# Optimization experiments

Hardware: AMD Instinct MI355X
Metric: run time of the kernel (lower is better)

The kernel has to match this reference:

```python
import jax, jax.numpy as jnp
import numpy as np

B, K, C = 8192, 64, 8  # batch, feature dim, number of private-attribute classes


def setup_inputs() -> dict:
    key = jax.random.key(0)
    k1, k2, k3 = jax.random.split(key, 3)
    mu = jax.random.normal(k1, (B, K), dtype=jnp.float32)
    private_attribute = jax.random.randint(k2, (B,), 0, C)
    A = jax.random.normal(k3, (K, K), dtype=jnp.float32) * 0.05
    cov = A @ A.T + jnp.eye(K, dtype=jnp.float32)  # SPD prior covariance
    return {"mu": mu, "private_attribute": private_attribute, "cov": cov}


def _kldiv(mu1, S1, mu2, S2, k):
    # KL( N(mu1,S1) || N(mu2,S2) )
    d = mu2 - mu1
    tr = jnp.trace(jnp.linalg.solve(S2, S1))       # tr(inv(S2) S1)
    quad = d @ jnp.linalg.solve(S2, d)             # d^T inv(S2) d
    ld2 = jnp.linalg.slogdet(S2)[1]
    ld1 = jnp.linalg.slogdet(S1)[1]
    return 0.5 * (tr + quad - k + ld2 - ld1)


def reference(mu, private_attribute, cov):
    Bn, k = mu.shape
    labels = private_attribute
    ones = jnp.ones((Bn,), mu.dtype)
    counts = jax.ops.segment_sum(ones, labels, num_segments=C)                # [C]
    safe = jnp.maximum(counts, 1.0)
    mu_F = jax.ops.segment_sum(mu, labels, num_segments=C) / safe[:, None]    # [C,k] group means
    mu_total = jnp.mean(mu, axis=0)                                           # [k]
    dt = mu - mu_total
    Sigma_total = cov + dt.T @ dt / Bn                                        # [k,k]
    dc = mu - mu_F[labels]                                                    # [B,k]
    outer = jnp.einsum('bi,bj->bij', dc, dc)                                  # [B,k,k]
    Sigma_F = cov + jax.ops.segment_sum(outer, labels, num_segments=C) / safe[:, None, None]  # [C,k,k]
    kl = jax.vmap(lambda m, S: _kldiv(m, S, mu_total, Sigma_total, k))(mu_F, Sigma_F)  # [C]
    # The original loops `for i in range(len(keys)-1)` over dict keys ordered by
    # first occurrence in the batch, i.e. it SKIPS the class whose first sample
    # appears latest. Reproduce that exactly.
    pos = jnp.arange(Bn)
    first_pos = jnp.min(
        jnp.where(labels[:, None] == jnp.arange(C)[None, :], pos[:, None], Bn), axis=0
    )                                                                          # [C]
    present = first_pos < Bn
    last_key = jnp.argmax(jnp.where(present, first_pos, -1))
    w = jnp.where(present & (jnp.arange(C) != last_key), counts, 0.0)          # count_Fs weights
    result = jnp.sum(kl * w * Bn) / (Bn ** 2)
    return result
```

## Files before the change

kernel.cpp:

```cpp
#include <hip/hip_runtime.h>

#define CC 8
#define KK 64
#define BB 8192
#define NCHUNK 16
#define ROWS_PER_CHUNK (BB / NCHUNK)

#define OFF_G       0
#define OFF_GSUM    262144
#define OFF_GCOUNT  264192
#define OFF_GFIRST  264224
#define OFF_INV     264256
#define OFF_LOG     297024
#define OFF_L       297096
#define OFF_LDI     329864
#define OFF_X       330376
#define OFF_GPART   363144

__global__ __launch_bounds__(256) void gram_stats_kernel(
    const float* __restrict__ mu, const int* __restrict__ labels,
    float* __restrict__ Gpart, float* __restrict__ gsum,
    int* __restrict__ gcount, int* __restrict__ gfirst) {
  int c = blockIdx.y;
  int chunk = blockIdx.x;
  int tid = threadIdx.x;
  int lane = tid & 63, w = tid >> 6;
  int tx = tid & 15, ty = tid >> 4;
  __shared__ float rows[64][KK];
  __shared__ int labs[64];
  __shared__ float ssum[KK];
  double acc[4][4] = {{0.0}};
  float rsum = 0.f;
  int cnt = 0, first = BB;
  int base = chunk * ROWS_PER_CHUNK;
  const float4* mu4 = (const float4*)mu + (size_t)base * (KK / 4);

  if (tid < KK) ssum[tid] = 0.f;

  float4 pf[4];
  int plab = 0;
#pragma unroll
  for (int i = 0; i < 4; ++i) pf[i] = mu4[tid + i * 256];
  if (tid < 64) plab = labels[base + tid];

#pragma unroll 1
  for (int g = 0; g < ROWS_PER_CHUNK / 64; ++g) {
    __syncthreads();
    float4* rows4 = (float4*)&rows[0][0];
#pragma unroll
    for (int i = 0; i < 4; ++i) rows4[tid + i * 256] = pf[i];
    if (tid < 64) labs[tid] = plab;
    __syncthreads();
    if (g + 1 < ROWS_PER_CHUNK / 64) {
#pragma unroll
      for (int i = 0; i < 4; ++i) pf[i] = mu4[(g + 1) * 1024 + tid + i * 256];
      if (tid < 64) plab = labels[base + (g + 1) * 64 + tid];
    }
#pragma unroll 4
    for (int r = 0; r < 16; ++r) {
      int rr = w * 16 + r;
      if (labs[rr] == c) rsum += rows[rr][lane];
    }
    if (lane < 16 && labs[w * 16 + lane] == c) {
      cnt++;
      first = min(first, base + g * 64 + w * 16 + lane);
    }
    unsigned long long m = __ballot(labs[lane] == c);
    while (m) {
      int r = __builtin_ctzll(m);
      m &= m - 1;
      const float4* rw4 = (const float4*)rows[r];
      float4 a4 = rw4[ty], b4 = rw4[tx];
      const float* ai = (const float*)&a4;
      const float* bj = (const float*)&b4;
#pragma unroll
      for (int a = 0; a < 4; ++a)
#pragma unroll
        for (int b = 0; b < 4; ++b) acc[a][b] += (double)ai[a] * (double)bj[b];
    }
  }
  float* Gp = Gpart + ((size_t)chunk * CC + c) * KK * KK;
#pragma unroll
  for (int a = 0; a < 4; ++a)
#pragma unroll
    for (int b = 0; b < 4; ++b)
      Gp[(ty * 4 + a) * KK + tx * 4 + b] = (float)acc[a][b];
  atomicAdd(&ssum[lane], rsum);
  __syncthreads();
  if (tid < KK) {
    float v = ssum[tid];
    if (v != 0.f) atomicAdd(&gsum[c * KK + tid], v);
  }
  if (lane < 16) {
#pragma unroll
    for (int off = 8; off; off >>= 1) {
      cnt += __shfl_down(cnt, off);
      first = min(first, __shfl_down(first, off));
    }
    if (lane == 0 && cnt) {
      atomicAdd(&gcount[c], cnt);
      atomicMin(&gfirst[c], first);
    }
  }
}

__global__ __launch_bounds__(256) void greduce_kernel(
    const float* __restrict__ Gpart, double* __restrict__ G) {
  int c = blockIdx.y;
  int e = blockIdx.x * 256 + threadIdx.x;
  double s = 0.0;
#pragma unroll
  for (int p = 0; p < NCHUNK; ++p)
    s += (double)Gpart[((size_t)p * CC + c) * KK * KK + e];
  G[(size_t)c * KK * KK + e] = s;
}

__global__ __launch_bounds__(64) void factor_kernel(
    const double* __restrict__ G, const float* __restrict__ cov,
    const float* __restrict__ gsum, const int* __restrict__ gcount,
    double* __restrict__ logdets, double* __restrict__ Lg,
    double* __restrict__ Ldig, float* __restrict__ out) {
  int blk = blockIdx.x;
  int t = threadIdx.x;
  __shared__ double bufA[KK][KK + 1];
  __shared__ double bufB[KK][KK + 1];
  __shared__ double panelb[8][KK];
  __shared__ double mb[KK];

  bool isS2 = (blk == CC);
  if (isS2 && t == 0) out[0] = 0.f;

  double safe = 1.0, ncd = 0.0;
  if (!isS2) {
    int nc = gcount[blk];
    ncd = (double)nc;
    safe = nc > 0 ? ncd : 1.0;
    mb[t] = (double)gsum[blk * KK + t] / safe;
  } else {
    double s = 0.0;
#pragma unroll
    for (int c = 0; c < CC; ++c) s += (double)gsum[c * KK + t];
    mb[t] = s / (double)BB;
  }
  double mt = mb[t];

  if (!isS2) {
    const double* Gc = G + (size_t)blk * KK * KK;
    double inv_safe = 1.0 / safe;
#pragma unroll 8
    for (int j = 0; j < KK; ++j)
      bufA[t][j] = (double)cov[j * KK + t] + (Gc[j * KK + t] - ncd * mt * mb[j]) * inv_safe;
  } else {
    const double invB = 1.0 / (double)BB;
#pragma unroll 4
    for (int j = 0; j < KK; ++j) {
      double g = 0.0;
#pragma unroll
      for (int c = 0; c < CC; ++c) g += G[(size_t)c * KK * KK + j * KK + t];
      bufA[t][j] = (double)cov[j * KK + t] + g * invB - mt * mb[j];
    }
  }

  double (*cur)[KK + 1] = bufA;
  double (*nxt)[KK + 1] = bufB;
  double ldacc = 0.0;
  int bound = t | 7;
#pragma unroll 1
  for (int p = 0; p < 8; ++p) {
    int P0 = p * 8;
    double cc_[8];
#pragma unroll
    for (int m = 0; m < 8; ++m) cc_[m] = cur[t][P0 + m];
    double uu[8];
    double pd = 1.0;
#pragma unroll
    for (int m = 0; m < 8; ++m) {
      double akk = __shfl(cc_[m], P0 + m);
      pd *= akk;
      double inv;
      asm("v_rcp_f64 %0, %1" : "=v"(inv) : "v"(akk));
      inv = inv * fma(-akk, inv, 2.0);
      inv = inv * fma(-akk, inv, 2.0);
      uu[m] = cc_[m] * inv;
      panelb[m][t] = cc_[m];
      if (isS2) {
        double rsv = sqrt(akk) * inv;
        Lg[(P0 + m) * KK + t] = cc_[m] * rsv;
        if (t == 0) Ldig[P0 + m] = rsv;
      }
#pragma unroll
      for (int mm = m + 1; mm < 8; ++mm)
        cc_[mm] -= uu[m] * __shfl(cc_[m], P0 + mm);
    }
    ldacc += log(pd);
#pragma unroll 1
    for (int j = P0 + 8; j < KK; j += 8) {
      if (j <= bound) {
        double aj[8];
#pragma unroll
        for (int q = 0; q < 8; ++q) aj[q] = cur[t][j + q];
#pragma unroll
        for (int m = 0; m < 8; ++m)
#pragma unroll
          for (int q = 0; q < 8; ++q)
            aj[q] -= uu[m] * panelb[m][j + q];
#pragma unroll
        for (int q = 0; q < 8; ++q) nxt[t][j + q] = aj[q];
      }
    }
    { auto tmp = cur; cur = nxt; nxt = tmp; }
  }
  if (t == 0) logdets[blk] = ldacc;
}

__global__ __launch_bounds__(64) void solve_kernel(
    const double* __restrict__ Lg, const double* __restrict__ Ldig,
    double* __restrict__ Xg) {
  int t = threadIdx.x;
  __shared__ double Lt[KK][KK];
  __shared__ double Xs[KK][KK];
  __shared__ double Ldi[KK];
#pragma unroll 8
  for (int j = 0; j < KK; ++j) Lt[j][t] = Lg[j * KK + t];
  Ldi[t] = Ldig[t];
  __syncthreads();

#pragma unroll 1
  for (int g = 0; g < 8; ++g) {
    int I0 = g * 8;
    double sv[8], ldl[8];
#pragma unroll
    for (int m = 0; m < 8; ++m) { sv[m] = 0.0; ldl[m] = Ldi[I0 + m]; }
#pragma unroll 4
    for (int j = 0; j < I0; ++j) {
      double xj = Xs[j][t];
#pragma unroll
      for (int m = 0; m < 8; ++m) sv[m] += Lt[j][I0 + m] * xj;
    }
#pragma unroll
    for (int m = 0; m < 8; ++m) {
      int i = I0 + m;
      double x = (((i == t) ? 1.0 : 0.0) - sv[m]) * ldl[m];
#pragma unroll
      for (int mm = m + 1; mm < 8; ++mm) sv[mm] += Lt[i][I0 + mm] * x;
      Xs[i][t] = x;
    }
  }
  __syncthreads();
#pragma unroll 8
  for (int i = 0; i < KK; ++i) Xg[i * KK + t] = Xs[i][t];
}

__global__ __launch_bounds__(64) void xtx_kernel(
    const double* __restrict__ Xg, double* __restrict__ invS2) {
  int b = blockIdx.x;
  int t = threadIdx.x;
  __shared__ double Xs[KK][KK];
#pragma unroll 8
  for (int k = 0; k < KK; ++k) Xs[k][t] = Xg[k * KK + t];
  __syncthreads();
#pragma unroll 1
  for (int rr = 0; rr < 8; ++rr) {
    int r = b + rr * 8;
    double s = 0.0;
#pragma unroll 4
    for (int k = r; k < KK; ++k) s += Xs[k][r] * Xs[k][t];
    invS2[r * KK + t] = s;
  }
}

__global__ __launch_bounds__(64) void combine_kernel(
    const double* __restrict__ G, const double* __restrict__ invS2,
    const double* __restrict__ logdets, const float* __restrict__ cov,
    const int* __restrict__ gcount, const int* __restrict__ gfirst,
    const float* __restrict__ gsum, float* __restrict__ out) {
  int c = blockIdx.x;
  int t = threadIdx.x;
  __shared__ double mv[KK];
  __shared__ double dv[KK];

  double mtot;
  {
    double s = 0.0;
#pragma unroll
    for (int cc2 = 0; cc2 < CC; ++cc2) s += (double)gsum[cc2 * KK + t];
    mtot = s / (double)BB;
  }
  int nc = gcount[c];
  double safe = nc > 0 ? (double)nc : 1.0;
  double mt = (double)gsum[c * KK + t] / safe;
  double dt = mtot - mt;
  mv[t] = mt;
  dv[t] = dt;

  const double* Gc = G + (size_t)c * KK * KK;
  double tg = 0.0, qm = 0.0, qd = 0.0, tic = 0.0;
#pragma unroll 4
  for (int m = 0; m < KK; ++m) {
    double w = invS2[m * KK + t];
    tic += w * (double)cov[m * KK + t];
    tg += w * Gc[m * KK + t];
    qm += w * mv[m];
    qd += w * dv[m];
  }
  qm *= mt;
  qd *= dt;
#pragma unroll
  for (int m = 32; m; m >>= 1) {
    tg += __shfl_down(tg, m);
    qm += __shfl_down(qm, m);
    qd += __shfl_down(qd, m);
    tic += __shfl_down(tic, m);
  }
  if (t == 0) {
    int best = 0;
    long long bv = -2;
    for (int cc2 = 0; cc2 < CC; ++cc2) {
      long long v = gcount[cc2] > 0 ? (long long)gfirst[cc2] : -1;
      if (v > bv) { bv = v; best = cc2; }
    }
    double tr = tic + (tg - (double)nc * qm) / safe;
    double kl = 0.5 * (tr + qd - (double)KK + logdets[CC] - logdets[c]);
    double w = (nc > 0 && c != best) ? (double)nc : 0.0;
    atomicAdd(out, (float)(kl * w / (double)BB));
  }
}

extern "C" void kernel_launch(void* const* d_in, const int* in_sizes, int n_in,
                              void* d_out, int out_size, void* d_ws, size_t ws_size,
                              hipStream_t stream) {
  (void)in_sizes; (void)n_in; (void)out_size; (void)ws_size;
  const float* mu = (const float*)d_in[0];
  const int* labels = (const int*)d_in[1];
  const float* cov = (const float*)d_in[2];
  float* out = (float*)d_out;
  char* ws = (char*)d_ws;

  double* G = (double*)(ws + OFF_G);
  float* gsum = (float*)(ws + OFF_GSUM);
  int* gcount = (int*)(ws + OFF_GCOUNT);
  int* gfirst = (int*)(ws + OFF_GFIRST);
  double* invS2 = (double*)(ws + OFF_INV);
  double* logdets = (double*)(ws + OFF_LOG);
  double* Lg = (double*)(ws + OFF_L);
  double* Ldig = (double*)(ws + OFF_LDI);
  double* Xg = (double*)(ws + OFF_X);
  float* Gpart = (float*)(ws + OFF_GPART);

  hipMemsetAsync(ws + OFF_GSUM, 0, OFF_GFIRST - OFF_GSUM, stream);
  hipMemsetAsync(ws + OFF_GFIRST, 0x7f, CC * sizeof(int), stream);

  gram_stats_kernel<<<dim3(NCHUNK, CC), 256, 0, stream>>>(mu, labels, Gpart, gsum, gcount, gfirst);
  greduce_kernel<<<dim3(16, CC), 256, 0, stream>>>(Gpart, G);
  factor_kernel<<<CC + 1, 64, 0, stream>>>(G, cov, gsum, gcount, logdets, Lg, Ldig, out);
  solve_kernel<<<1, 64, 0, stream>>>(Lg, Ldig, Xg);
  xtx_kernel<<<CC, 64, 0, stream>>>(Xg, invS2);
  combine_kernel<<<CC, 64, 0, stream>>>(G, invS2, logdets, cov, gcount, gfirst, gsum, out);
}
```

Baseline: 117.2 us.

## Fuse triangular solve and inverse product into factor kernel with 256 threads

```diff
diff --git a/kernel.cpp b/kernel.cpp
--- a/kernel.cpp
+++ b/kernel.cpp
@@ -7,15 +7,20 @@
 #define ROWS_PER_CHUNK (BB / NCHUNK)
 
 #define OFF_G       0
-#define OFF_GSUM    262144
-#define OFF_GCOUNT  264192
-#define OFF_GFIRST  264224
-#define OFF_INV     264256
-#define OFF_LOG     297024
-#define OFF_L       297096
-#define OFF_LDI     329864
-#define OFF_X       330376
-#define OFF_GPART   363144
+#define OFF_GSUM    294912
+#define OFF_GCOUNT  296960
+#define OFF_GFIRST  296992
+#define OFF_INV     297024
+#define OFF_LOG     329792
+#define OFF_GPART   329864
+
+__device__ __forceinline__ double readlane_f64(double v, int lane) {
+  union { double d; int i[2]; } u, r;
+  u.d = v;
+  r.i[0] = __builtin_amdgcn_readlane(u.i[0], lane);
+  r.i[1] = __builtin_amdgcn_readlane(u.i[1], lane);
+  return r.d;
+}
 
 __global__ __launch_bounds__(256) void gram_stats_kernel(
     const float* __restrict__ mu, const int* __restrict__ labels,
@@ -109,65 +114,75 @@
   int c = blockIdx.y;
   int e = blockIdx.x * 256 + threadIdx.x;
   double s = 0.0;
-#pragma unroll
-  for (int p = 0; p < NCHUNK; ++p)
-    s += (double)Gpart[((size_t)p * CC + c) * KK * KK + e];
+  if (c < CC) {
+#pragma unroll
+    for (int p = 0; p < NCHUNK; ++p)
+      s += (double)Gpart[((size_t)p * CC + c) * KK * KK + e];
+  } else {
+#pragma unroll 4
+    for (int p = 0; p < NCHUNK; ++p)
+#pragma unroll
+      for (int c2 = 0; c2 < CC; ++c2)
+        s += (double)Gpart[((size_t)p * CC + c2) * KK * KK + e];
+  }
   G[(size_t)c * KK * KK + e] = s;
 }
 
-__global__ __launch_bounds__(64) void factor_kernel(
+__global__ __launch_bounds__(256) void factor_kernel(
     const double* __restrict__ G, const float* __restrict__ cov,
     const float* __restrict__ gsum, const int* __restrict__ gcount,
-    double* __restrict__ logdets, double* __restrict__ Lg,
-    double* __restrict__ Ldig, float* __restrict__ out) {
+    double* __restrict__ logdets, double* __restrict__ invS2,
+    float* __restrict__ out) {
   int blk = blockIdx.x;
-  int t = threadIdx.x;
+  int tid = threadIdx.x;
+  int t = tid & 63;
+  int w = tid >> 6;
   __shared__ double bufA[KK][KK + 1];
   __shared__ double bufB[KK][KK + 1];
   __shared__ double panelb[8][KK];
+  __shared__ double Lb[KK][KK + 1];
+  __shared__ double Ldi[KK];
   __shared__ double mb[KK];
 
   bool isS2 = (blk == CC);
-  if (isS2 && t == 0) out[0] = 0.f;
-
-  double safe = 1.0, ncd = 0.0;
+  if (isS2 && tid == 0) out[0] = 0.f;
+
+  double safe, ncd, mt;
   if (!isS2) {
     int nc = gcount[blk];
     ncd = (double)nc;
     safe = nc > 0 ? ncd : 1.0;
-    mb[t] = (double)gsum[blk * KK + t] / safe;
+    mt = (double)gsum[blk * KK + t] / safe;
   } else {
+    ncd = (double)BB;
+    safe = (double)BB;
     double s = 0.0;
 #pragma unroll
     for (int c = 0; c < CC; ++c) s += (double)gsum[c * KK + t];
-    mb[t] = s / (double)BB;
-  }
-  double mt = mb[t];
-
-  if (!isS2) {
+    mt = s / safe;
+  }
+  if (w == 0) mb[t] = mt;
+  __syncthreads();
+
+  {
     const double* Gc = G + (size_t)blk * KK * KK;
     double inv_safe = 1.0 / safe;
-#pragma unroll 8
-    for (int j = 0; j < KK; ++j)
+    int j0 = w * 16;
+#pragma unroll 4
+    for (int jj = 0; jj < 16; ++jj) {
+      int j = j0 + jj;
       bufA[t][j] = (double)cov[j * KK + t] + (Gc[j * KK + t] - ncd * mt * mb[j]) * inv_safe;
-  } else {
-    const double invB = 1.0 / (double)BB;
-#pragma unroll 4
-    for (int j = 0; j < KK; ++j) {
-      double g = 0.0;
-#pragma unroll
-      for (int c = 0; c < CC; ++c) g += G[(size_t)c * KK * KK + j * KK + t];
-      bufA[t][j] = (double)cov[j * KK + t] + g * invB - mt * mb[j];
-    }
-  }
+    }
+  }
+  __syncthreads();
 
   double (*cur)[KK + 1] = bufA;
   double (*nxt)[KK + 1] = bufB;
   double ldacc = 0.0;
   int bound = t | 7;
-#pragma unroll 1
+#pragma unroll
   for (int p = 0; p < 8; ++p) {
-    int P0 = p * 8;
+    const int P0 = p * 8;
     double cc_[8];
 #pragma unroll
     for (int m = 0; m < 8; ++m) cc_[m] = cur[t][P0 + m];
@@ -175,26 +190,30 @@
     double pd = 1.0;
 #pragma unroll
     for (int m = 0; m < 8; ++m) {
-      double akk = __shfl(cc_[m], P0 + m);
+      double akk = readlane_f64(cc_[m], P0 + m);
       pd *= akk;
       double inv;
       asm("v_rcp_f64 %0, %1" : "=v"(inv) : "v"(akk));
       inv = inv * fma(-akk, inv, 2.0);
       inv = inv * fma(-akk, inv, 2.0);
       uu[m] = cc_[m] * inv;
-      panelb[m][t] = cc_[m];
-      if (isS2) {
-        double rsv = sqrt(akk) * inv;
-        Lg[(P0 + m) * KK + t] = cc_[m] * rsv;
-        if (t == 0) Ldig[P0 + m] = rsv;
+      if (w == 0) {
+        panelb[m][t] = cc_[m];
+        if (isS2) {
+          double rsv = sqrt(akk) * inv;
+          Lb[t][P0 + m] = cc_[m] * rsv;
+          if (t == 0) Ldi[P0 + m] = rsv;
+        }
       }
 #pragma unroll
       for (int mm = m + 1; mm < 8; ++mm)
-        cc_[mm] -= uu[m] * __shfl(cc_[m], P0 + mm);
+        cc_[mm] -= uu[m] * readlane_f64(cc_[m], P0 + mm);
     }
     ldacc += log(pd);
+    __syncthreads();
 #pragma unroll 1
-    for (int j = P0 + 8; j < KK; j += 8) {
+    for (int jb = p + 1 + w; jb < 8; jb += 4) {
+      int j = jb * 8;
       if (j <= bound) {
         double aj[8];
 #pragma unroll
@@ -208,64 +227,45 @@
         for (int q = 0; q < 8; ++q) nxt[t][j + q] = aj[q];
       }
     }
+    __syncthreads();
     { auto tmp = cur; cur = nxt; nxt = tmp; }
   }
-  if (t == 0) logdets[blk] = ldacc;
-}
-
-__global__ __launch_bounds__(64) void solve_kernel(
-    const double* __restrict__ Lg, const double* __restrict__ Ldig,
-    double* __restrict__ Xg) {
-  int t = threadIdx.x;
-  __shared__ double Lt[KK][KK];
-  __shared__ double Xs[KK][KK];
-  __shared__ double Ldi[KK];
-#pragma unroll 8
-  for (int j = 0; j < KK; ++j) Lt[j][t] = Lg[j * KK + t];
-  Ldi[t] = Ldig[t];
-  __syncthreads();
-
+  if (tid == 0) logdets[blk] = ldacc;
+
+  if (isS2) {
+    double (*Xs)[KK] = (double (*)[KK])(&bufA[0][0]);
+    if (w == 0) {
 #pragma unroll 1
-  for (int g = 0; g < 8; ++g) {
-    int I0 = g * 8;
-    double sv[8], ldl[8];
-#pragma unroll
-    for (int m = 0; m < 8; ++m) { sv[m] = 0.0; ldl[m] = Ldi[I0 + m]; }
-#pragma unroll 4
-    for (int j = 0; j < I0; ++j) {
-      double xj = Xs[j][t];
-#pragma unroll
-      for (int m = 0; m < 8; ++m) sv[m] += Lt[j][I0 + m] * xj;
-    }
-#pragma unroll
-    for (int m = 0; m < 8; ++m) {
-      int i = I0 + m;
-      double x = (((i == t) ? 1.0 : 0.0) - sv[m]) * ldl[m];
-#pragma unroll
-      for (int mm = m + 1; mm < 8; ++mm) sv[mm] += Lt[i][I0 + mm] * x;
-      Xs[i][t] = x;
-    }
-  }
-  __syncthreads();
-#pragma unroll 8
-  for (int i = 0; i < KK; ++i) Xg[i * KK + t] = Xs[i][t];
-}
-
-__global__ __launch_bounds__(64) void xtx_kernel(
-    const double* __restrict__ Xg, double* __restrict__ invS2) {
-  int b = blockIdx.x;
-  int t = threadIdx.x;
-  __shared__ double Xs[KK][KK];
-#pragma unroll 8
-  for (int k = 0; k < KK; ++k) Xs[k][t] = Xg[k * KK + t];
-  __syncthreads();
+      for (int g = 0; g < 8; ++g) {
+        int I0 = g * 8;
+        double sv[8];
+#pragma unroll
+        for (int m = 0; m < 8; ++m) sv[m] = 0.0;
+#pragma unroll 2
+        for (int j = 0; j < I0; ++j) {
+          double xj = Xs[j][t];
+#pragma unroll
+          for (int m = 0; m < 8; ++m) sv[m] += Lb[I0 + m][j] * xj;
+        }
+#pragma unroll
+        for (int m = 0; m < 8; ++m) {
+          int i = I0 + m;
+          double x = (((i == t) ? 1.0 : 0.0) - sv[m]) * Ldi[i];
+#pragma unroll
+          for (int mm = m + 1; mm < 8; ++mm) sv[mm] += Lb[I0 + mm][i] * x;
+          Xs[i][t] = x;
+        }
+      }
+    }
+    __syncthreads();
 #pragma unroll 1
-  for (int rr = 0; rr < 8; ++rr) {
-    int r = b + rr * 8;
-    double s = 0.0;
-#pragma unroll 4
-    for (int k = r; k < KK; ++k) s += Xs[k][r] * Xs[k][t];
-    invS2[r * KK + t] = s;
+    for (int rr = 0; rr < 16; ++rr) {
+      int r = w + rr * 4;
+      double s = 0.0;
+#pragma unroll 2
+      for (int k = r; k < KK; ++k) s += Xs[k][r] * Xs[k][t];
+      invS2[r * KK + t] = s;
+    }
   }
 }
 
@@ -321,8 +321,8 @@
     }
     double tr = tic + (tg - (double)nc * qm) / safe;
     double kl = 0.5 * (tr + qd - (double)KK + logdets[CC] - logdets[c]);
-    double w = (nc > 0 && c != best) ? (double)nc : 0.0;
-    atomicAdd(out, (float)(kl * w / (double)BB));
+    double wgt = (nc > 0 && c != best) ? (double)nc : 0.0;
+    atomicAdd(out, (float)(kl * wgt / (double)BB));
   }
 }
 
@@ -342,18 +342,13 @@
   int* gfirst = (int*)(ws + OFF_GFIRST);
   double* invS2 = (double*)(ws + OFF_INV);
   double* logdets = (double*)(ws + OFF_LOG);
-  double* Lg = (double*)(ws + OFF_L);
-  double* Ldig = (double*)(ws + OFF_LDI);
-  double* Xg = (double*)(ws + OFF_X);
   float* Gpart = (float*)(ws + OFF_GPART);
 
   hipMemsetAsync(ws + OFF_GSUM, 0, OFF_GFIRST - OFF_GSUM, stream);
   hipMemsetAsync(ws + OFF_GFIRST, 0x7f, CC * sizeof(int), stream);
 
   gram_stats_kernel<<<dim3(NCHUNK, CC), 256, 0, stream>>>(mu, labels, Gpart, gsum, gcount, gfirst);
-  greduce_kernel<<<dim3(16, CC), 256, 0, stream>>>(Gpart, G);
-  factor_kernel<<<CC + 1, 64, 0, stream>>>(G, cov, gsum, gcount, logdets, Lg, Ldig, out);
-  solve_kernel<<<1, 64, 0, stream>>>(Lg, Ldig, Xg);
-  xtx_kernel<<<CC, 64, 0, stream>>>(Xg, invS2);
+  greduce_kernel<<<dim3(16, CC + 1), 256, 0, stream>>>(Gpart, G);
+  factor_kernel<<<CC + 1, 256, 0, stream>>>(G, cov, gsum, gcount, logdets, invS2, out);
   combine_kernel<<<CC, 64, 0, stream>>>(G, invS2, logdets, cov, gcount, gfirst, gsum, out);
 }
```

Result: faster. 107.9 us (-8.0%).
